# Optimization experiments

Hardware: AMD Instinct MI355X
Metric: run time of the kernel (lower is better)

Reference implementation:

```python
import jax, jax.numpy as jnp
import numpy as np

# Constants from the module definition / init args
TOP_M = 10      # args.top_m
HEADS = 4       # nn.MultiheadAttention(512, 4)
EMBED = 512
HEAD_DIM = EMBED // HEADS


def setup_inputs() -> dict:
    key = jax.random.key(0)
    ks = jax.random.split(key, 6)
    B, T, N, C = 16, 60, 196, 512
    visual_patch_top_k = jax.random.normal(ks[0], (B, T, N, C), dtype=jnp.float32)
    qst_feat = jax.random.normal(ks[1], (B, C), dtype=jnp.float32)
    s = 0.02
    # q/k slices of nn.MultiheadAttention's packed in_proj (v/out_proj/FFN/LN do not
    # affect the module's returned outputs, which depend only on attention weights)
    Wq = jax.random.normal(ks[2], (C, C), dtype=jnp.float32) * s
    bq = jnp.zeros((C,), dtype=jnp.float32)
    Wk = jax.random.normal(ks[3], (C, C), dtype=jnp.float32) * s
    bk = jnp.zeros((C,), dtype=jnp.float32)
    return {"visual_patch_top_k": visual_patch_top_k, "qst_feat": qst_feat,
            "Wq": Wq, "bq": bq, "Wk": Wk, "bk": bk}


def reference(visual_patch_top_k, qst_feat, Wq, bq, Wk, bk):
    B, T, N, C = visual_patch_top_k.shape
    # --- soft_attention_select_3d: batched over T (original loops frame-by-frame) ---
    # q: [B, H, Dh] single query token per batch element
    q = (qst_feat @ Wq.T + bq).reshape(B, HEADS, HEAD_DIM)
    # k: [B, T, N, H, Dh]
    k = (jnp.einsum('btnc,ec->btne', visual_patch_top_k, Wk) + bk
         ).reshape(B, T, N, HEADS, HEAD_DIM)
    scale = 1.0 / jnp.sqrt(jnp.float32(HEAD_DIM))
    scores = jnp.einsum('bhd,btnhd->bhtn', q, k) * scale  # [B, H, T, N]
    attn = jax.nn.softmax(scores, axis=-1)
    # torch MHA returns head-averaged weights; query length is 1
    patch_weights = attn.mean(axis=1)                      # [B, T, N]

    # --- find_top_m (faithful to the original, including its gather bug) ---
    sort_index = jnp.argsort(patch_weights, axis=-1)       # ascending by weight
    top_m_index = sort_index[..., -TOP_M:]                 # top-m patch ids
    top_m_index_sort = jnp.sort(top_m_index, axis=-1)      # ascending by index
    # Original nested loop iterates only top_m_index_sort[0][0] and overwrites the
    # full [:, :] slab each iteration -> only the LAST (largest) index of batch 0,
    # frame 0 survives, broadcast over all (b, t, m).
    p = top_m_index_sort[0, 0, -1]
    sel = jnp.take(visual_patch_top_k, p, axis=2)          # [B, T, C]
    visual_patch_top_m = jnp.broadcast_to(sel[:, :, None, :], (B, T, TOP_M, C))
    visual_patch_feat = visual_patch_top_m.reshape(B, T * TOP_M, C)
    return (visual_patch_top_m, visual_patch_feat)
```

## Files before the change

### kernel.cpp

```cpp
#include <hip/hip_runtime.h>
#include <math.h>

#define BB 16
#define TT 60
#define NN 196
#define CC 512
#define HH 4
#define DD 128
#define TOPM 10
#define NPG 49
#define SCALE 0.08838834764831845f

__global__ void __launch_bounds__(256) k_front(
        const float* __restrict__ x, const float* __restrict__ qst,
        const float* __restrict__ Wq, const float* __restrict__ bq,
        const float* __restrict__ Wk, float* __restrict__ sp) {
    __shared__ float  qs[8];
    __shared__ float4 upart[2][128];
    __shared__ float4 u4[128];

    int b = blockIdx.x, t = threadIdx.x;
    int h = b & 3, dg = (b >> 2) & 15, ng = b >> 6;
    int row0 = h * DD + dg * 8;

    {
        int r = t >> 5, l = t & 31;
        const float4* wrow = (const float4*)(Wq + (size_t)(row0 + r) * CC);
        const float4* qv4  = (const float4*)qst;
        float acc = 0.f;
#pragma unroll
        for (int j = 0; j < 4; ++j) {
            float4 w = wrow[l + 32 * j], v = qv4[l + 32 * j];
            acc += w.x * v.x + w.y * v.y + w.z * v.z + w.w * v.w;
        }
#pragma unroll
        for (int off = 16; off; off >>= 1) acc += __shfl_xor(acc, off, 32);
        if (l == 0) qs[r] = (acc + bq[row0 + r]) * SCALE;
    }
    __syncthreads();

    {
        int c4 = t & 127, half = t >> 7;
        float4 a = make_float4(0.f, 0.f, 0.f, 0.f);
#pragma unroll
        for (int i = 0; i < 4; ++i) {
            int r = half * 4 + i;
            float qv = qs[r];
            float4 w = ((const float4*)Wk)[(size_t)(row0 + r) * 128 + c4];
            a.x += qv * w.x; a.y += qv * w.y; a.z += qv * w.z; a.w += qv * w.w;
        }
        upart[half][c4] = a;
    }
    __syncthreads();
    if (t < 128) {
        float4 a = upart[0][t], bb = upart[1][t];
        u4[t] = make_float4(a.x + bb.x, a.y + bb.y, a.z + bb.z, a.w + bb.w);
    }
    __syncthreads();

    {
        int wv = t >> 6, lane = t & 63;
        float4 ua = u4[lane * 2], ub = u4[lane * 2 + 1];
        for (int i = wv; i < NPG; i += 4) {
            int n = ng * NPG + i;
            const float4* xr = (const float4*)(x + (size_t)n * CC);
            float4 xa = xr[lane * 2], xb = xr[lane * 2 + 1];
            float acc = xa.x * ua.x + xa.y * ua.y + xa.z * ua.z + xa.w * ua.w +
                        xb.x * ub.x + xb.y * ub.y + xb.z * ub.z + xb.w * ub.w;
#pragma unroll
            for (int off = 32; off; off >>= 1) acc += __shfl_xor(acc, off);
            if (lane == 0) sp[(h * 16 + dg) * NN + n] = acc;
        }
    }
}

__global__ void __launch_bounds__(256) k_bcast_sel(
        const float* __restrict__ x, const float* __restrict__ sp,
        float* __restrict__ out) {
    __shared__ float att[HH][NN];
    __shared__ int spi;
    int t = threadIdx.x, wv = t >> 6, lane = t & 63;

    {
        const float* base = sp + wv * 16 * NN;
        float s0 = 0.f, s1 = 0.f, s2 = 0.f, s3 = 0.f;
#pragma unroll
        for (int dg = 0; dg < 16; ++dg) {
            const float* r = base + dg * NN;
            s0 += r[lane]; s1 += r[lane + 64]; s2 += r[lane + 128];
            if (lane < 4) s3 += r[lane + 192];
        }
        float s3m = (lane < 4) ? s3 : -1e30f;
        float m = fmaxf(fmaxf(s0, s1), fmaxf(s2, s3m));
#pragma unroll
        for (int off = 32; off; off >>= 1) m = fmaxf(m, __shfl_xor(m, off));
        float e0 = expf(s0 - m), e1 = expf(s1 - m), e2 = expf(s2 - m);
        float e3 = (lane < 4) ? expf(s3 - m) : 0.f;
        float ss = e0 + e1 + e2 + e3;
#pragma unroll
        for (int off = 32; off; off >>= 1) ss += __shfl_xor(ss, off);
        float inv = 1.f / ss;
        att[wv][lane] = e0 * inv;
        att[wv][lane + 64] = e1 * inv;
        att[wv][lane + 128] = e2 * inv;
        if (lane < 4) att[wv][lane + 192] = e3 * inv;
    }
    __syncthreads();

    if (wv == 0) {
        float v0 = 0.25f * (att[0][lane] + att[1][lane] + att[2][lane] + att[3][lane]);
        float v1 = 0.25f * (att[0][lane + 64] + att[1][lane + 64] + att[2][lane + 64] + att[3][lane + 64]);
        float v2 = 0.25f * (att[0][lane + 128] + att[1][lane + 128] + att[2][lane + 128] + att[3][lane + 128]);
        float v3 = (lane < 4)
            ? 0.25f * (att[0][lane + 192] + att[1][lane + 192] + att[2][lane + 192] + att[3][lane + 192])
            : -2e30f;
        int p = -1;
        for (int r = 0; r < TOPM; ++r) {
            float v = -3e30f; int idx = -1;
            if (v0 >= v) { v = v0; idx = lane; }
            if (v1 >= v) { v = v1; idx = lane + 64; }
            if (v2 >= v) { v = v2; idx = lane + 128; }
            if (v3 >= v) { v = v3; idx = lane + 192; }
#pragma unroll
            for (int off = 32; off; off >>= 1) {
                float vo = __shfl_xor(v, off);
                int   io = __shfl_xor(idx, off);
                if (vo > v || (vo == v && io > idx)) { v = vo; idx = io; }
            }
            if ((idx & 63) == lane) {
                int jj = idx >> 6;
                if (jj == 0) v0 = -2e30f;
                else if (jj == 1) v1 = -2e30f;
                else if (jj == 2) v2 = -2e30f;
                else v3 = -2e30f;
            }
            if (idx > p) p = idx;
        }
        if (lane == 0) spi = p;
    }
    __syncthreads();
    int p = spi;

    int gt = blockIdx.x * 256 + t;
    int bt = gt >> 7;
    int c4 = gt & 127;
    float4 v = ((const float4*)x)[((size_t)bt * NN + p) * 128 + c4];
    float4* o0 = (float4*)out + ((size_t)bt * TOPM) * 128 + c4;
    float4* o1 = o0 + (size_t)BB * TT * TOPM * 128;
#pragma unroll
    for (int m = 0; m < TOPM; ++m) {
        o0[(size_t)m * 128] = v;
        o1[(size_t)m * 128] = v;
    }
}

extern "C" void kernel_launch(void* const* d_in, const int* in_sizes, int n_in,
                              void* d_out, int out_size, void* d_ws, size_t ws_size,
                              hipStream_t stream) {
    const float* x   = (const float*)d_in[0];
    const float* qst = (const float*)d_in[1];
    const float* Wq  = (const float*)d_in[2];
    const float* bq  = (const float*)d_in[3];
    const float* Wk  = (const float*)d_in[4];

    float* sp = (float*)d_ws;

    k_front    <<<256, 256, 0, stream>>>(x, qst, Wq, bq, Wk, sp);
    k_bcast_sel<<<(BB * TT * 128) / 256, 256, 0, stream>>>(x, sp, (float*)d_out);
}
```

Baseline: 33.16 us.

## Split selection into single-block kernel and copy with nontemporal stores

The per-block redundant softmax/top-m selection is moved into a separate single-block kernel that writes the selected patch index to workspace. A separate copy kernel reads that index and broadcasts the row using nontemporal stores. This removes duplicated selection work across all copy blocks and reduces cache pollution from the large output write, at the cost of an extra kernel launch and serialization.

New measurement: 32.23 us. 1.03x faster.

```diff
diff --git a/kernel.cpp b/kernel.cpp
--- a/kernel.cpp
+++ b/kernel.cpp
@@ -10,6 +10,10 @@
 #define TOPM 10
 #define NPG 49
 #define SCALE 0.08838834764831845f
+
+typedef float f32x4 __attribute__((ext_vector_type(4)));
+
+#define WS_P (HH * 16 * NN)
 
 __global__ void __launch_bounds__(256) k_front(
         const float* __restrict__ x, const float* __restrict__ qst,
@@ -74,11 +78,9 @@
     }
 }
 
-__global__ void __launch_bounds__(256) k_bcast_sel(
-        const float* __restrict__ x, const float* __restrict__ sp,
-        float* __restrict__ out) {
+__global__ void __launch_bounds__(256) k_select(
+        const float* __restrict__ sp, int* __restrict__ pOut) {
     __shared__ float att[HH][NN];
-    __shared__ int spi;
     int t = threadIdx.x, wv = t >> 6, lane = t & 63;
 
     {
@@ -136,21 +138,24 @@
             }
             if (idx > p) p = idx;
         }
-        if (lane == 0) spi = p;
+        if (lane == 0) *pOut = p;
     }
-    __syncthreads();
-    int p = spi;
+}
 
-    int gt = blockIdx.x * 256 + t;
+__global__ void __launch_bounds__(256) k_copy(
+        const float* __restrict__ x, const int* __restrict__ pPtr,
+        float* __restrict__ out) {
+    int p = *pPtr;
+    int gt = blockIdx.x * 256 + threadIdx.x;
     int bt = gt >> 7;
     int c4 = gt & 127;
-    float4 v = ((const float4*)x)[((size_t)bt * NN + p) * 128 + c4];
-    float4* o0 = (float4*)out + ((size_t)bt * TOPM) * 128 + c4;
-    float4* o1 = o0 + (size_t)BB * TT * TOPM * 128;
+    f32x4 v = ((const f32x4*)x)[((size_t)bt * NN + p) * 128 + c4];
+    f32x4* o0 = (f32x4*)out + ((size_t)bt * TOPM) * 128 + c4;
+    f32x4* o1 = o0 + (size_t)BB * TT * TOPM * 128;
 #pragma unroll
     for (int m = 0; m < TOPM; ++m) {
-        o0[(size_t)m * 128] = v;
-        o1[(size_t)m * 128] = v;
+        __builtin_nontemporal_store(v, o0 + (size_t)m * 128);
+        __builtin_nontemporal_store(v, o1 + (size_t)m * 128);
     }
 }
 
@@ -164,7 +169,9 @@
     const float* Wk  = (const float*)d_in[4];
 
     float* sp = (float*)d_ws;
+    int*   p  = (int*)(sp + WS_P);
 
-    k_front    <<<256, 256, 0, stream>>>(x, qst, Wq, bq, Wk, sp);
-    k_bcast_sel<<<(BB * TT * 128) / 256, 256, 0, stream>>>(x, sp, (float*)d_out);
+    k_front <<<256, 256, 0, stream>>>(x, qst, Wq, bq, Wk, sp);
+    k_select<<<1,   256, 0, stream>>>(sp, p);
+    k_copy  <<<(BB * TT * 128) / 256, 256, 0, stream>>>(x, p, (float*)d_out);
 }
```
